# Optimization experiments

Measured on AMD Instinct MI355X. Metric: run time of the kernel, lower is better.

Reference implementation:

```python
import jax, jax.numpy as jnp
import numpy as np

N_NODES = 50000
N_EDGES = 800000
D_IN, HIDDEN, OUT, K = 96, 64, 16, 3


def _glorot(key, shape):
    fan_in, fan_out = shape[-2], shape[-1]
    lim = (6.0 / (fan_in + fan_out)) ** 0.5
    return jax.random.uniform(key, shape, jnp.float32, -lim, lim)


def setup_inputs() -> dict:
    key = jax.random.key(0)
    k1, k2, k3, k4 = jax.random.split(key, 4)
    x = jax.random.normal(k1, (N_NODES, D_IN), dtype=jnp.float32)
    edge_index = jax.random.randint(k2, (2, N_EDGES), 0, N_NODES, dtype=jnp.int64)
    # ChebConv params: K stacked linear maps per layer + one bias per layer
    W1 = _glorot(k3, (K, D_IN, HIDDEN))
    b1 = jnp.zeros((HIDDEN,), jnp.float32)
    W2 = _glorot(k4, (K, HIDDEN, OUT))
    b2 = jnp.zeros((OUT,), jnp.float32)
    return {"x": x, "edge_index": edge_index, "W1": W1, "b1": b1, "W2": W2, "b2": b2}


def _cheb_norm(edge_index, num_nodes):
    # PyG ChebConv norm with normalization='sym', lambda_max=2.0:
    # Ltilde = (2/lmax)*(I - D^-1/2 A D^-1/2) - I = -D^-1/2 A D^-1/2 (diag weight 0)
    src, dst = edge_index[0], edge_index[1]
    ones = jnp.ones((edge_index.shape[1],), jnp.float32)
    deg = jax.ops.segment_sum(ones, src, num_segments=num_nodes)
    dis = jnp.where(deg > 0, jax.lax.rsqrt(jnp.maximum(deg, 1.0)), 0.0)
    return -dis[src] * dis[dst]  # [E]


def _cheb_conv(x, src, dst, w, W, b, num_nodes):
    # Chebyshev recurrence: Tx0=x, Tx1=L x, Txk=2 L Tx_{k-1} - Tx_{k-2}
    def prop(h):  # sparse matvec: scatter-add of weighted source features
        return jax.ops.segment_sum(w[:, None] * h[src], dst, num_segments=num_nodes)

    Tx0 = x
    out = Tx0 @ W[0]
    Tx1 = prop(Tx0)
    out = out + Tx1 @ W[1]
    for k in range(2, W.shape[0]):
        Tx2 = 2.0 * prop(Tx1) - Tx0
        out = out + Tx2 @ W[k]
        Tx0, Tx1 = Tx1, Tx2
    return out + b


def reference(x, edge_index, W1, b1, W2, b2):
    num_nodes = x.shape[0]
    src, dst = edge_index[0], edge_index[1]
    w = _cheb_norm(edge_index, num_nodes)
    h = jax.nn.relu(_cheb_conv(x, src, dst, w, W1, b1, num_nodes))
    return _cheb_conv(h, src, dst, w, W2, b2, num_nodes)
```

## Files before the change

kernel.cpp:

```cpp
#include <hip/hip_runtime.h>

#define N_NODES 50000
#define N_EDGES 800000
#define D_IN 96
#define HID 64
#define D_OUT 16

#define EPB 2048
#define NBLK_E ((N_EDGES + EPB - 1) / EPB)
#define BSHIFT 7
#define NBKT ((N_NODES + 127) / 128)
#define DCAP 2560
#define PACK_TOT (3 * D_IN * HID + 3 * HID * D_OUT)
#define PACK_BLKS (PACK_TOT / 256)
#define GEMM1_BLKS ((N_NODES / 16 + 3) / 4)

typedef unsigned short u16;
typedef unsigned int u32;
typedef __attribute__((ext_vector_type(4))) float f32x4;
typedef __attribute__((ext_vector_type(8))) short bf16x8;

__device__ inline float bflo(u32 v) { union { u32 i; float f; } u; u.i = v << 16; return u.f; }
__device__ inline float bfhi(u32 v) { union { u32 i; float f; } u; u.i = v & 0xffff0000u; return u.f; }
__device__ inline u16 f2bf(float f) {
    union { float f; u32 i; } u; u.f = f;
    return (u16)((u.i + 0x7fffu + ((u.i >> 16) & 1u)) >> 16);
}
__device__ inline u32 pack2(float lo, float hi) {
    return (u32)f2bf(lo) | ((u32)f2bf(hi) << 16);
}


__global__ __launch_bounds__(256)
void passA(const int* __restrict__ src, const int* __restrict__ dst,
           int* __restrict__ blk_cnt_src, int* __restrict__ blk_cnt_dst,
           const float* __restrict__ W1, const float* __restrict__ W2,
           u16* __restrict__ Pb1, u16* __restrict__ Pb2) {
    const int t = threadIdx.x, blk = blockIdx.x;
    if (blk >= NBLK_E) {
        int tt = (blk - NBLK_E) * 256 + t;
        if (tt < 3 * D_IN * HID) {
            int j = tt & 7, rest = tt >> 3;
            int c = rest % 192, i = (rest / 192) * 8 + j;
            int kc = c / 64, o = c % 64;
            Pb1[tt] = f2bf(W1[((long)kc * D_IN + i) * HID + o]);
        } else if (tt < PACK_TOT) {
            int t2 = tt - 3 * D_IN * HID;
            int j = t2 & 7, rest = t2 >> 3;
            int c = rest % 48, i = (rest / 48) * 8 + j;
            int kc = c / 16, o = c % 16;
            Pb2[t2] = f2bf(W2[((long)kc * HID + i) * D_OUT + o]);
        }
        return;
    }
    __shared__ int hs[NBKT], hd[NBKT];
    for (int i = t; i < NBKT; i += 256) { hs[i] = 0; hd[i] = 0; }
    __syncthreads();
    const int e0 = blk * EPB;
    const int e1 = (e0 + EPB < N_EDGES) ? e0 + EPB : N_EDGES;
    for (int e = e0 + t; e < e1; e += 256) {
        atomicAdd(&hs[src[e] >> BSHIFT], 1);
        atomicAdd(&hd[dst[e] >> BSHIFT], 1);
    }
    __syncthreads();
    for (int b = t; b < NBKT; b += 256) {
        blk_cnt_src[b * NBLK_E + blk] = hs[b];
        blk_cnt_dst[b * NBLK_E + blk] = hd[b];
    }
}

__global__ __launch_bounds__(64)
void passB(int* __restrict__ blk_cnt_src, int* __restrict__ blk_cnt_dst,
           int* __restrict__ tot_src, int* __restrict__ tot_dst) {
    const int b = blockIdx.x;
    int* cnt; int* tot;
    if (b < NBKT) { cnt = blk_cnt_dst + b * NBLK_E;          tot = tot_dst + b; }
    else          { cnt = blk_cnt_src + (b - NBKT) * NBLK_E; tot = tot_src + (b - NBKT); }
    const int lane = threadIdx.x;
    int carry = 0;
    for (int base0 = 0; base0 < NBLK_E; base0 += 64) {
        int i = base0 + lane;
        int v = (i < NBLK_E) ? cnt[i] : 0;
        int incl = v;
        #pragma unroll
        for (int off = 1; off < 64; off <<= 1) {
            int x = __shfl_up(incl, off);
            if (lane >= off) incl += x;
        }
        if (i < NBLK_E) cnt[i] = carry + incl - v;
        carry += __shfl(incl, 63);
    }
    if (lane == 0) *tot = carry;
}


template<int K, int NC, int LDZ, int CPK, bool AF32, bool SCALE>
__device__ __forceinline__
void gemm_body(int tile, int lane, const void* __restrict__ Av, const u16* sP,
               u16* __restrict__ D02, u16* __restrict__ Z1, u16* __restrict__ Z2out,
               const float* __restrict__ dis) {
    constexpr int KT = K / 32;
    const int node0 = tile * 16;
    const int sub = lane >> 4, r16 = lane & 15;
    float dis4[4];
    if constexpr (SCALE) {
        #pragma unroll
        for (int r = 0; r < 4; ++r) dis4[r] = dis[node0 + sub * 4 + r];
    }
    bf16x8 a[KT];
    if constexpr (AF32) {
        const float* ar = (const float*)Av + (long)(node0 + r16) * K + sub * 8;
        #pragma unroll
        for (int kt = 0; kt < KT; ++kt) {
            float4 a0 = *(const float4*)(ar + kt * 32);
            float4 a1 = *(const float4*)(ar + kt * 32 + 4);
            union { bf16x8 v; uint4 q; } u;
            u.q.x = pack2(a0.x, a0.y); u.q.y = pack2(a0.z, a0.w);
            u.q.z = pack2(a1.x, a1.y); u.q.w = pack2(a1.z, a1.w);
            a[kt] = u.v;
        }
    } else {
        const u16* ar = (const u16*)Av + (long)(node0 + r16) * K + sub * 8;
        #pragma unroll
        for (int kt = 0; kt < KT; ++kt)
            a[kt] = *(const bf16x8*)(ar + kt * 32);
    }
    auto cc = [&](int ct) {
        f32x4 acc = {0.f, 0.f, 0.f, 0.f};
        #pragma unroll
        for (int kt = 0; kt < KT; ++kt) {
            bf16x8 bfr = *(const bf16x8*)&sP[((kt * 4 + sub) * NC + ct * 16 + r16) * 8];
            acc = __builtin_amdgcn_mfma_f32_16x16x32_bf16(a[kt], bfr, acc, 0, 0, 0);
        }
        return acc;
    };
    #pragma unroll
    for (int i = 0; i < CPK; ++i) {
        f32x4 acc0 = cc(i);
        f32x4 acc2 = cc(2 * CPK + i);
        const long rowoff = (long)(node0 + sub * 4) * LDZ + i * 16 + r16;
        #pragma unroll
        for (int r = 0; r < 4; ++r) {
            D02[rowoff + (long)r * LDZ] = f2bf(acc0[r] - acc2[r]);
            Z2out[rowoff + (long)r * LDZ] = SCALE ? f2bf(acc2[r] * dis4[r]) : f2bf(acc2[r]);
        }
    }
    #pragma unroll
    for (int i = 0; i < CPK; ++i) {
        f32x4 acc1 = cc(CPK + i);
        const long rowoff = (long)(node0 + sub * 4) * LDZ + i * 16 + r16;
        #pragma unroll
        for (int r = 0; r < 4; ++r)
            Z1[rowoff + (long)r * LDZ] = f2bf(acc1[r]);
    }
}


__global__ __launch_bounds__(256)
void passC_gemm1(const int* __restrict__ src, const int* __restrict__ dst,
                 const int* __restrict__ blk_off_src, const int* __restrict__ blk_off_dst,
                 const int* __restrict__ tot_src, const int* __restrict__ tot_dst,
                 u16* __restrict__ sorted_srconly, u32* __restrict__ sorted_pair,
                 const float* __restrict__ x, const u16* __restrict__ Pb1,
                 u16* __restrict__ D02, u16* __restrict__ Z1, u16* __restrict__ Zs) {
    __shared__ __align__(16) char smem[36864];
    const int t = threadIdx.x, blk = blockIdx.x;
    if (blk >= NBLK_E) {
        u16* sP = (u16*)smem;
        for (int idx = t * 8; idx < D_IN * 192; idx += 2048)
            *(uint4*)&sP[idx] = *(const uint4*)&Pb1[idx];
        __syncthreads();
        const int tile = (blk - NBLK_E) * 4 + (t >> 6);
        if (tile * 16 >= N_NODES) return;
        gemm_body<D_IN, 192, HID, 4, true, false>(tile, t & 63, x, sP, D02, Z1, Zs, nullptr);
        return;
    }
    int* s  = (int*)smem;
    int* cs = s + 512;
    int* cd = cs + NBKT;
    for (int pass = 0; pass < 2; ++pass) {
        const int* tot = pass ? tot_src : tot_dst;
        const int* bo  = pass ? blk_off_src : blk_off_dst;
        int* cx = pass ? cs : cd;
        s[t]       = (t < NBKT) ? tot[t] : 0;
        s[t + 256] = (t + 256 < NBKT) ? tot[t + 256] : 0;
        __syncthreads();
        for (int off = 1; off < 512; off <<= 1) {
            int a1 = (t >= off) ? s[t - off] : 0;
            int a2 = (t + 256 >= off) ? s[t + 256 - off] : 0;
            __syncthreads();
            s[t] += a1; s[t + 256] += a2;
            __syncthreads();
        }
        if (t < NBKT) cx[t] = s[t] - tot[t] + bo[t * NBLK_E + blk];
        if (t + 256 < NBKT) cx[t + 256] = s[t + 256] - tot[t + 256] + bo[(t + 256) * NBLK_E + blk];
        __syncthreads();
    }
    const int e0 = blk * EPB;
    const int e1 = (e0 + EPB < N_EDGES) ? e0 + EPB : N_EDGES;
    for (int e = e0 + t; e < e1; e += 256) {
        int sv = src[e], dv = dst[e];
        int ps = atomicAdd(&cs[sv >> BSHIFT], 1);
        sorted_srconly[ps] = (u16)sv;
        int pd = atomicAdd(&cd[dv >> BSHIFT], 1);
        sorted_pair[pd] = ((u32)dv << 16) | (u32)sv;
    }
}

__global__ __launch_bounds__(256)
void passD(const int* __restrict__ tot_src, const u16* __restrict__ sorted_srconly,
           const int* __restrict__ tot_dst, const u32* __restrict__ sorted_pair,
           float* __restrict__ dis, int* __restrict__ row_ptr, u16* __restrict__ wsrc,
           u16* __restrict__ Zs) {
    __shared__ int sred[256];
    __shared__ int hist[128];
    __shared__ int cur[128];
    __shared__ float s_dis[128];
    __shared__ u32 s_p[DCAP];
    const int t = threadIdx.x;
    const bool isSrc = blockIdx.x < NBKT;
    const int b = isSrc ? blockIdx.x : blockIdx.x - NBKT;
    const int* tot = isSrc ? tot_src : tot_dst;
    int part = 0;
    for (int i = t; i < b; i += 256) part += tot[i];
    sred[t] = part;
    if (t < 128) hist[t] = 0;
    __syncthreads();
    #pragma unroll
    for (int off = 128; off > 0; off >>= 1) {
        if (t < off) sred[t] += sred[t + off];
        __syncthreads();
    }
    const int eb = sred[0];
    const int ee = eb + tot[b];
    if (isSrc) {
        for (int i = eb + t; i < ee; i += 256)
            atomicAdd(&hist[sorted_srconly[i] & 127], 1);
        __syncthreads();
        const int node0 = b << BSHIFT;
        if (t < 128) {
            int c = hist[t];
            float dv = c > 0 ? rsqrtf((float)c) : 0.0f;
            s_dis[t] = dv;
            if (node0 + t < N_NODES) dis[node0 + t] = dv;
        }
        __syncthreads();
        for (int c = t; c < 128 * 8; c += 256) {
            int ln = c >> 3, off8 = (c & 7) * 8;
            int n = node0 + ln;
            if (n >= N_NODES) continue;
            float dv = s_dis[ln];
            u16* zp = Zs + (long)n * HID + off8;
            uint4 q = *(uint4*)zp;
            uint4 r;
            r.x = pack2(bflo(q.x) * dv, bfhi(q.x) * dv);
            r.y = pack2(bflo(q.y) * dv, bfhi(q.y) * dv);
            r.z = pack2(bflo(q.z) * dv, bfhi(q.z) * dv);
            r.w = pack2(bflo(q.w) * dv, bfhi(q.w) * dv);
            *(uint4*)zp = r;
        }
        return;
    }
    if (b == 0 && t == 0) row_ptr[N_NODES] = N_EDGES;
    const int cnt = ee - eb;
    const int stage = cnt < DCAP ? cnt : DCAP;
    for (int i = t; i < stage; i += 256) {
        u32 v = sorted_pair[eb + i];
        s_p[i] = v;
        atomicAdd(&hist[(v >> 16) & 127], 1);
    }
    for (int i = stage + t; i < cnt; i += 256)
        atomicAdd(&hist[(sorted_pair[eb + i] >> 16) & 127], 1);
    __syncthreads();
    if (t < 64) {
        int v0 = hist[2 * t], v1 = hist[2 * t + 1];
        int p = v0 + v1;
        int incl = p;
        #pragma unroll
        for (int off = 1; off < 64; off <<= 1) {
            int x = __shfl_up(incl, off);
            if (t >= off) incl += x;
        }
        int excl = incl - p;
        cur[2 * t] = excl;
        cur[2 * t + 1] = excl + v0;
        int node = (b << BSHIFT) + 2 * t;
        if (node < N_NODES) row_ptr[node] = eb + excl;
        if (node + 1 < N_NODES) row_ptr[node + 1] = eb + excl + v0;
    }
    __syncthreads();
    for (int i = t; i < stage; i += 256) {
        u32 v = s_p[i];
        int slot = atomicAdd(&cur[(v >> 16) & 127], 1);
        wsrc[eb + slot] = (u16)(v & 0xFFFF);
    }
    for (int i = stage + t; i < cnt; i += 256) {
        u32 v = sorted_pair[eb + i];
        int slot = atomicAdd(&cur[(v >> 16) & 127], 1);
        wsrc[eb + slot] = (u16)(v & 0xFFFF);
    }
}


__global__ __launch_bounds__(256)
void gemm2_kernel(const u16* __restrict__ A, const u16* __restrict__ P,
                  u16* __restrict__ D02, u16* __restrict__ Z1, u16* __restrict__ Zs,
                  const float* __restrict__ dis) {
    __shared__ u16 sP[HID * 48];
    for (int idx = threadIdx.x * 8; idx < HID * 48; idx += 2048)
        *(uint4*)&sP[idx] = *(const uint4*)&P[idx];
    __syncthreads();
    const int tile = blockIdx.x * 4 + (threadIdx.x >> 6);
    if (tile * 16 >= N_NODES) return;
    gemm_body<HID, 48, D_OUT, 1, false, true>(tile, threadIdx.x & 63, A, sP, D02, Z1, Zs, dis);
}


#define EPI_S 0
#define EPI_H 1
#define EPI_OUT 2

__device__ inline void sum8(float (&acc)[8], uint4 q) {
    acc[0] += bflo(q.x); acc[1] += bfhi(q.x);
    acc[2] += bflo(q.y); acc[3] += bfhi(q.y);
    acc[4] += bflo(q.z); acc[5] += bfhi(q.z);
    acc[6] += bflo(q.w); acc[7] += bfhi(q.w);
}

template<int F, int FS, int NPB, int CAP, int EPI>
__global__ __launch_bounds__(256)
void gather_prop(const int* __restrict__ row_ptr, const u16* __restrict__ ws,
                 const u16* __restrict__ g,
                 const u16* __restrict__ aux1,
                 const float* __restrict__ bias,
                 const float* __restrict__ dis,
                 void* __restrict__ outp) {
    static_assert(NPB * (FS / 8) == 256, "block geometry");
    constexpr int SPLIT = F / FS;
    __shared__ u16 s_p[CAP];
    __shared__ int s_beg[NPB + 1];
    const int tid = threadIdx.x;
    const int nodeblk = blockIdx.x / SPLIT;
    const int half = blockIdx.x % SPLIT;
    const int node0 = nodeblk * NPB;
    if (tid <= NPB) {
        int n = node0 + tid;
        s_beg[tid] = row_ptr[n > N_NODES ? N_NODES : n];
    }
    __syncthreads();
    const int ebeg = s_beg[0];
    const int cnt = s_beg[NPB] - ebeg;
    const int stage = cnt < CAP ? cnt : CAP;
    for (int e = tid; e < stage; e += 256)
        s_p[e] = ws[ebeg + e];
    __syncthreads();
    constexpr int CPN = FS / 8;
    const int nl = tid / CPN;
    const int node = node0 + nl;
    if (node >= N_NODES) return;
    const int c8 = (tid % CPN) * 8 + half * FS;
    float acc[8];
    #pragma unroll
    for (int j = 0; j < 8; ++j) acc[j] = 0.0f;
    const int beg = s_beg[nl] - ebeg;
    const int end = s_beg[nl + 1] - ebeg;
    const int mid = end < stage ? end : stage;
    int e = beg;
    for (; e + 8 <= mid; e += 8) {
        int p0 = s_p[e],     p1 = s_p[e + 1], p2 = s_p[e + 2], p3 = s_p[e + 3];
        int p4 = s_p[e + 4], p5 = s_p[e + 5], p6 = s_p[e + 6], p7 = s_p[e + 7];
        uint4 q0 = *(const uint4*)(g + (long)p0 * F + c8);
        uint4 q1 = *(const uint4*)(g + (long)p1 * F + c8);
        uint4 q2 = *(const uint4*)(g + (long)p2 * F + c8);
        uint4 q3 = *(const uint4*)(g + (long)p3 * F + c8);
        uint4 q4 = *(const uint4*)(g + (long)p4 * F + c8);
        uint4 q5 = *(const uint4*)(g + (long)p5 * F + c8);
        uint4 q6 = *(const uint4*)(g + (long)p6 * F + c8);
        uint4 q7 = *(const uint4*)(g + (long)p7 * F + c8);
        sum8(acc, q0); sum8(acc, q1); sum8(acc, q2); sum8(acc, q3);
        sum8(acc, q4); sum8(acc, q5); sum8(acc, q6); sum8(acc, q7);
    }
    for (; e + 4 <= mid; e += 4) {
        int p0 = s_p[e], p1 = s_p[e + 1], p2 = s_p[e + 2], p3 = s_p[e + 3];
        uint4 q0 = *(const uint4*)(g + (long)p0 * F + c8);
        uint4 q1 = *(const uint4*)(g + (long)p1 * F + c8);
        uint4 q2 = *(const uint4*)(g + (long)p2 * F + c8);
        uint4 q3 = *(const uint4*)(g + (long)p3 * F + c8);
        sum8(acc, q0); sum8(acc, q1); sum8(acc, q2); sum8(acc, q3);
    }
    for (; e < mid; ++e)
        sum8(acc, *(const uint4*)(g + (long)s_p[e] * F + c8));
    for (e = (beg > stage ? beg : stage); e < end; ++e)
        sum8(acc, *(const uint4*)(g + (long)ws[ebeg + e] * F + c8));
    const float dd = dis[node];
    if (EPI == EPI_S) {
        const float m1 = dd, m2 = -2.0f * dd * dd;
        const uint4 z1 = *(const uint4*)(aux1 + (long)node * F + c8);
        uint4 r;
        r.x = pack2(fmaf(m1, bflo(z1.x), m2 * acc[0]), fmaf(m1, bfhi(z1.x), m2 * acc[1]));
        r.y = pack2(fmaf(m1, bflo(z1.y), m2 * acc[2]), fmaf(m1, bfhi(z1.y), m2 * acc[3]));
        r.z = pack2(fmaf(m1, bflo(z1.z), m2 * acc[4]), fmaf(m1, bfhi(z1.z), m2 * acc[5]));
        r.w = pack2(fmaf(m1, bflo(z1.w), m2 * acc[6]), fmaf(m1, bfhi(z1.w), m2 * acc[7]));
        *(uint4*)((u16*)outp + (long)node * F + c8) = r;
    } else {
        const uint4 z0 = *(const uint4*)(aux1 + (long)node * F + c8);
        const float* bb = bias + c8;
        float v0 = bflo(z0.x) - dd * acc[0] + bb[0];
        float v1 = bfhi(z0.x) - dd * acc[1] + bb[1];
        float v2 = bflo(z0.y) - dd * acc[2] + bb[2];
        float v3 = bfhi(z0.y) - dd * acc[3] + bb[3];
        float v4 = bflo(z0.z) - dd * acc[4] + bb[4];
        float v5 = bfhi(z0.z) - dd * acc[5] + bb[5];
        float v6 = bflo(z0.w) - dd * acc[6] + bb[6];
        float v7 = bfhi(z0.w) - dd * acc[7] + bb[7];
        if (EPI == EPI_H) {
            uint4 r;
            r.x = pack2(fmaxf(v0, 0.f), fmaxf(v1, 0.f));
            r.y = pack2(fmaxf(v2, 0.f), fmaxf(v3, 0.f));
            r.z = pack2(fmaxf(v4, 0.f), fmaxf(v5, 0.f));
            r.w = pack2(fmaxf(v6, 0.f), fmaxf(v7, 0.f));
            *(uint4*)((u16*)outp + (long)node * F + c8) = r;
        } else {
            float* op = (float*)outp + (long)node * F + c8;
            *(float4*)op = make_float4(v0, v1, v2, v3);
            *(float4*)(op + 4) = make_float4(v4, v5, v6, v7);
        }
    }
}


extern "C" void kernel_launch(void* const* d_in, const int* in_sizes, int n_in,
                              void* d_out, int out_size, void* d_ws, size_t ws_size,
                              hipStream_t stream) {
    const float* x  = (const float*)d_in[0];
    const int*   ei = (const int*)d_in[1];
    const float* W1 = (const float*)d_in[2];
    const float* b1 = (const float*)d_in[3];
    const float* W2 = (const float*)d_in[4];
    const float* b2 = (const float*)d_in[5];
    const int* src = ei;
    const int* dst = ei + N_EDGES;

    float* dis          = (float*)d_ws;
    int*   row_ptr      = (int*)(dis + N_NODES);
    int*   blk_cnt_src  = row_ptr + 50016;
    int*   blk_cnt_dst  = blk_cnt_src + 152896;
    int*   tot_src      = blk_cnt_dst + 152896;
    int*   tot_dst      = tot_src + 512;
    u16*   srconly      = (u16*)(tot_dst + 512);
    u32*   sorted_pair  = (u32*)(srconly + N_EDGES);
    u16*   wsrc         = (u16*)(sorted_pair + N_EDGES);
    u16*   D02          = wsrc + N_EDGES;
    u16*   Z1b          = D02 + (long)N_NODES * HID;
    u16*   Zs           = Z1b + (long)N_NODES * HID;
    u16*   S            = Zs  + (long)N_NODES * HID;
    u16*   hb           = S   + (long)N_NODES * HID;
    u16*   D02p         = hb  + (long)N_NODES * HID;
    u16*   Z1p          = D02p + (long)N_NODES * D_OUT;
    u16*   Zsp          = Z1p  + (long)N_NODES * D_OUT;
    u16*   Sp           = Zsp  + (long)N_NODES * D_OUT;
    u16*   Pb1          = Sp   + (long)N_NODES * D_OUT;
    u16*   Pb2          = Pb1 + 18432;

    passA<<<NBLK_E + PACK_BLKS, 256, 0, stream>>>(src, dst, blk_cnt_src, blk_cnt_dst,
                                                  W1, W2, Pb1, Pb2);
    passB<<<2 * NBKT, 64, 0, stream>>>(blk_cnt_src, blk_cnt_dst, tot_src, tot_dst);
    passC_gemm1<<<NBLK_E + GEMM1_BLKS, 256, 0, stream>>>(
        src, dst, blk_cnt_src, blk_cnt_dst, tot_src, tot_dst,
        srconly, sorted_pair, x, Pb1, D02, Z1b, Zs);
    passD<<<2 * NBKT, 256, 0, stream>>>(tot_src, srconly, tot_dst, sorted_pair,
                                        dis, row_ptr, wsrc, Zs);

    gather_prop<HID, 32, 64, 1536, EPI_S><<<2 * ((N_NODES + 63) / 64), 256, 0, stream>>>(
        row_ptr, wsrc, Zs, Z1b, nullptr, dis, S);
    gather_prop<HID, 32, 64, 1536, EPI_H><<<2 * ((N_NODES + 63) / 64), 256, 0, stream>>>(
        row_ptr, wsrc, S, D02, b1, dis, hb);

    gemm2_kernel<<<GEMM1_BLKS, 256, 0, stream>>>(hb, Pb2, D02p, Z1p, Zsp, dis);
    gather_prop<D_OUT, 16, 128, 3072, EPI_S><<<(N_NODES + 127) / 128, 256, 0, stream>>>(
        row_ptr, wsrc, Zsp, Z1p, nullptr, dis, Sp);
    gather_prop<D_OUT, 16, 128, 3072, EPI_OUT><<<(N_NODES + 127) / 128, 256, 0, stream>>>(
        row_ptr, wsrc, Sp, D02p, b2, dis, (float*)d_out);
}
```

Measured before the change: 120.5 us.

## Fuse second layer-1 propagation with ReLU and layer-2 GEMM via LDS tile

The gather that produces the ReLU hidden features now keeps each 32-node tile of h in shared memory and immediately runs the layer-2 MFMA GEMM on it, writing D02p/Z1p/Zsp directly. This removes the separate gemm2 kernel launch and the global write and read of the 50000x64 bf16 hidden tensor. In exchange the gather uses 32 nodes per block with all 64 features instead of 64 nodes split across two blocks, only two of four waves do the GEMM, and LDS use per block rises, which may lower occupancy.

Result: faster. 117.7 us (-2.4%).

```diff
diff --git a/kernel.cpp b/kernel.cpp
--- a/kernel.cpp
+++ b/kernel.cpp
@@ -94,19 +94,13 @@
 }
 
 
-template<int K, int NC, int LDZ, int CPK, bool AF32, bool SCALE>
+template<int K, int NC, int LDZ, int CPK, bool AF32>
 __device__ __forceinline__
 void gemm_body(int tile, int lane, const void* __restrict__ Av, const u16* sP,
-               u16* __restrict__ D02, u16* __restrict__ Z1, u16* __restrict__ Z2out,
-               const float* __restrict__ dis) {
+               u16* __restrict__ D02, u16* __restrict__ Z1, u16* __restrict__ Z2out) {
     constexpr int KT = K / 32;
     const int node0 = tile * 16;
     const int sub = lane >> 4, r16 = lane & 15;
-    float dis4[4];
-    if constexpr (SCALE) {
-        #pragma unroll
-        for (int r = 0; r < 4; ++r) dis4[r] = dis[node0 + sub * 4 + r];
-    }
     bf16x8 a[KT];
     if constexpr (AF32) {
         const float* ar = (const float*)Av + (long)(node0 + r16) * K + sub * 8;
@@ -142,7 +136,7 @@
         #pragma unroll
         for (int r = 0; r < 4; ++r) {
             D02[rowoff + (long)r * LDZ] = f2bf(acc0[r] - acc2[r]);
-            Z2out[rowoff + (long)r * LDZ] = SCALE ? f2bf(acc2[r] * dis4[r]) : f2bf(acc2[r]);
+            Z2out[rowoff + (long)r * LDZ] = f2bf(acc2[r]);
         }
     }
     #pragma unroll
@@ -172,7 +166,7 @@
         __syncthreads();
         const int tile = (blk - NBLK_E) * 4 + (t >> 6);
         if (tile * 16 >= N_NODES) return;
-        gemm_body<D_IN, 192, HID, 4, true, false>(tile, t & 63, x, sP, D02, Z1, Zs, nullptr);
+        gemm_body<D_IN, 192, HID, 4, true>(tile, t & 63, x, sP, D02, Z1, Zs);
         return;
     }
     int* s  = (int*)smem;
@@ -302,24 +296,6 @@
 }
 
 
-__global__ __launch_bounds__(256)
-void gemm2_kernel(const u16* __restrict__ A, const u16* __restrict__ P,
-                  u16* __restrict__ D02, u16* __restrict__ Z1, u16* __restrict__ Zs,
-                  const float* __restrict__ dis) {
-    __shared__ u16 sP[HID * 48];
-    for (int idx = threadIdx.x * 8; idx < HID * 48; idx += 2048)
-        *(uint4*)&sP[idx] = *(const uint4*)&P[idx];
-    __syncthreads();
-    const int tile = blockIdx.x * 4 + (threadIdx.x >> 6);
-    if (tile * 16 >= N_NODES) return;
-    gemm_body<HID, 48, D_OUT, 1, false, true>(tile, threadIdx.x & 63, A, sP, D02, Z1, Zs, dis);
-}
-
-
-#define EPI_S 0
-#define EPI_H 1
-#define EPI_OUT 2
-
 __device__ inline void sum8(float (&acc)[8], uint4 q) {
     acc[0] += bflo(q.x); acc[1] += bfhi(q.x);
     acc[2] += bflo(q.y); acc[3] += bfhi(q.y);
@@ -327,44 +303,10 @@
     acc[6] += bflo(q.w); acc[7] += bfhi(q.w);
 }
 
-template<int F, int FS, int NPB, int CAP, int EPI>
-__global__ __launch_bounds__(256)
-void gather_prop(const int* __restrict__ row_ptr, const u16* __restrict__ ws,
-                 const u16* __restrict__ g,
-                 const u16* __restrict__ aux1,
-                 const float* __restrict__ bias,
-                 const float* __restrict__ dis,
-                 void* __restrict__ outp) {
-    static_assert(NPB * (FS / 8) == 256, "block geometry");
-    constexpr int SPLIT = F / FS;
-    __shared__ u16 s_p[CAP];
-    __shared__ int s_beg[NPB + 1];
-    const int tid = threadIdx.x;
-    const int nodeblk = blockIdx.x / SPLIT;
-    const int half = blockIdx.x % SPLIT;
-    const int node0 = nodeblk * NPB;
-    if (tid <= NPB) {
-        int n = node0 + tid;
-        s_beg[tid] = row_ptr[n > N_NODES ? N_NODES : n];
-    }
-    __syncthreads();
-    const int ebeg = s_beg[0];
-    const int cnt = s_beg[NPB] - ebeg;
-    const int stage = cnt < CAP ? cnt : CAP;
-    for (int e = tid; e < stage; e += 256)
-        s_p[e] = ws[ebeg + e];
-    __syncthreads();
-    constexpr int CPN = FS / 8;
-    const int nl = tid / CPN;
-    const int node = node0 + nl;
-    if (node >= N_NODES) return;
-    const int c8 = (tid % CPN) * 8 + half * FS;
-    float acc[8];
-    #pragma unroll
-    for (int j = 0; j < 8; ++j) acc[j] = 0.0f;
-    const int beg = s_beg[nl] - ebeg;
-    const int end = s_beg[nl + 1] - ebeg;
-    const int mid = end < stage ? end : stage;
+template<int F>
+__device__ __forceinline__
+void gather_loop(float (&acc)[8], const u16* s_p, const u16* ws, const u16* g,
+                 int beg, int mid, int end, int stage, int ebeg, int c8) {
     int e = beg;
     for (; e + 8 <= mid; e += 8) {
         int p0 = s_p[e],     p1 = s_p[e + 1], p2 = s_p[e + 2], p3 = s_p[e + 3];
@@ -392,6 +334,49 @@
         sum8(acc, *(const uint4*)(g + (long)s_p[e] * F + c8));
     for (e = (beg > stage ? beg : stage); e < end; ++e)
         sum8(acc, *(const uint4*)(g + (long)ws[ebeg + e] * F + c8));
+}
+
+
+#define EPI_S 0
+#define EPI_OUT 2
+
+template<int F, int FS, int NPB, int CAP, int EPI>
+__global__ __launch_bounds__(256)
+void gather_prop(const int* __restrict__ row_ptr, const u16* __restrict__ ws,
+                 const u16* __restrict__ g, const u16* __restrict__ aux1,
+                 const float* __restrict__ bias, const float* __restrict__ dis,
+                 void* __restrict__ outp) {
+    static_assert(NPB * (FS / 8) == 256, "block geometry");
+    constexpr int SPLIT = F / FS;
+    __shared__ u16 s_p[CAP];
+    __shared__ int s_beg[NPB + 1];
+    const int tid = threadIdx.x;
+    const int nodeblk = blockIdx.x / SPLIT;
+    const int half = blockIdx.x % SPLIT;
+    const int node0 = nodeblk * NPB;
+    if (tid <= NPB) {
+        int n = node0 + tid;
+        s_beg[tid] = row_ptr[n > N_NODES ? N_NODES : n];
+    }
+    __syncthreads();
+    const int ebeg = s_beg[0];
+    const int cnt = s_beg[NPB] - ebeg;
+    const int stage = cnt < CAP ? cnt : CAP;
+    for (int e = tid; e < stage; e += 256)
+        s_p[e] = ws[ebeg + e];
+    __syncthreads();
+    constexpr int CPN = FS / 8;
+    const int nl = tid / CPN;
+    const int node = node0 + nl;
+    if (node >= N_NODES) return;
+    const int c8 = (tid % CPN) * 8 + half * FS;
+    float acc[8];
+    #pragma unroll
+    for (int j = 0; j < 8; ++j) acc[j] = 0.0f;
+    const int beg = s_beg[nl] - ebeg;
+    const int end = s_beg[nl + 1] - ebeg;
+    const int mid = end < stage ? end : stage;
+    gather_loop<F>(acc, s_p, ws, g, beg, mid, end, stage, ebeg, c8);
     const float dd = dis[node];
     if (EPI == EPI_S) {
         const float m1 = dd, m2 = -2.0f * dd * dd;
@@ -413,18 +398,101 @@
         float v5 = bfhi(z0.z) - dd * acc[5] + bb[5];
         float v6 = bflo(z0.w) - dd * acc[6] + bb[6];
         float v7 = bfhi(z0.w) - dd * acc[7] + bb[7];
-        if (EPI == EPI_H) {
-            uint4 r;
-            r.x = pack2(fmaxf(v0, 0.f), fmaxf(v1, 0.f));
-            r.y = pack2(fmaxf(v2, 0.f), fmaxf(v3, 0.f));
-            r.z = pack2(fmaxf(v4, 0.f), fmaxf(v5, 0.f));
-            r.w = pack2(fmaxf(v6, 0.f), fmaxf(v7, 0.f));
-            *(uint4*)((u16*)outp + (long)node * F + c8) = r;
-        } else {
-            float* op = (float*)outp + (long)node * F + c8;
-            *(float4*)op = make_float4(v0, v1, v2, v3);
-            *(float4*)(op + 4) = make_float4(v4, v5, v6, v7);
-        }
+        float* op = (float*)outp + (long)node * F + c8;
+        *(float4*)op = make_float4(v0, v1, v2, v3);
+        *(float4*)(op + 4) = make_float4(v4, v5, v6, v7);
+    }
+}
+
+
+__global__ __launch_bounds__(256)
+void prop2_gemm2(const int* __restrict__ row_ptr, const u16* __restrict__ ws,
+                 const u16* __restrict__ S, const u16* __restrict__ D02,
+                 const float* __restrict__ b1, const float* __restrict__ dis,
+                 const u16* __restrict__ Pb2,
+                 u16* __restrict__ D02p, u16* __restrict__ Z1p, u16* __restrict__ Zsp) {
+    constexpr int NPB = 32, CAP = 1280;
+    __shared__ u16 s_p[CAP];
+    __shared__ int s_beg[NPB + 1];
+    __shared__ u16 sP[HID * 48];
+    __shared__ u16 h_tile[NPB][HID + 8];
+    const int tid = threadIdx.x;
+    const int node0 = blockIdx.x * NPB;
+    for (int idx = tid * 8; idx < HID * 48; idx += 2048)
+        *(uint4*)&sP[idx] = *(const uint4*)&Pb2[idx];
+    if (tid <= NPB) {
+        int n = node0 + tid;
+        s_beg[tid] = row_ptr[n > N_NODES ? N_NODES : n];
+    }
+    __syncthreads();
+    const int ebeg = s_beg[0];
+    const int cnt = s_beg[NPB] - ebeg;
+    const int stage = cnt < CAP ? cnt : CAP;
+    for (int e = tid; e < stage; e += 256)
+        s_p[e] = ws[ebeg + e];
+    __syncthreads();
+    const int nl = tid >> 3;
+    const int node = node0 + nl;
+    const int c8 = (tid & 7) * 8;
+    if (node < N_NODES) {
+        float acc[8];
+        #pragma unroll
+        for (int j = 0; j < 8; ++j) acc[j] = 0.0f;
+        const int beg = s_beg[nl] - ebeg;
+        const int end = s_beg[nl + 1] - ebeg;
+        const int mid = end < stage ? end : stage;
+        gather_loop<HID>(acc, s_p, ws, S, beg, mid, end, stage, ebeg, c8);
+        const float dd = dis[node];
+        const uint4 z0 = *(const uint4*)(D02 + (long)node * HID + c8);
+        const float* bb = b1 + c8;
+        float v0 = bflo(z0.x) - dd * acc[0] + bb[0];
+        float v1 = bfhi(z0.x) - dd * acc[1] + bb[1];
+        float v2 = bflo(z0.y) - dd * acc[2] + bb[2];
+        float v3 = bfhi(z0.y) - dd * acc[3] + bb[3];
+        float v4 = bflo(z0.z) - dd * acc[4] + bb[4];
+        float v5 = bfhi(z0.z) - dd * acc[5] + bb[5];
+        float v6 = bflo(z0.w) - dd * acc[6] + bb[6];
+        float v7 = bfhi(z0.w) - dd * acc[7] + bb[7];
+        uint4 r;
+        r.x = pack2(fmaxf(v0, 0.f), fmaxf(v1, 0.f));
+        r.y = pack2(fmaxf(v2, 0.f), fmaxf(v3, 0.f));
+        r.z = pack2(fmaxf(v4, 0.f), fmaxf(v5, 0.f));
+        r.w = pack2(fmaxf(v6, 0.f), fmaxf(v7, 0.f));
+        *(uint4*)&h_tile[nl][c8] = r;
+    }
+    __syncthreads();
+    const int w = tid >> 6;
+    if (w >= 2) return;
+    const int tile = blockIdx.x * 2 + w;
+    if (tile * 16 >= N_NODES) return;
+    const int lane = tid & 63;
+    const int sub = lane >> 4, r16 = lane & 15;
+    const int gnode0 = tile * 16;
+    float dis4[4];
+    #pragma unroll
+    for (int r = 0; r < 4; ++r) dis4[r] = dis[gnode0 + sub * 4 + r];
+    bf16x8 a[2];
+    const u16* ar = &h_tile[w * 16 + r16][sub * 8];
+    a[0] = *(const bf16x8*)(ar);
+    a[1] = *(const bf16x8*)(ar + 32);
+    auto cc = [&](int ct) {
+        f32x4 acc = {0.f, 0.f, 0.f, 0.f};
+        #pragma unroll
+        for (int kt = 0; kt < 2; ++kt) {
+            bf16x8 bfr = *(const bf16x8*)&sP[((kt * 4 + sub) * 48 + ct * 16 + r16) * 8];
+            acc = __builtin_amdgcn_mfma_f32_16x16x32_bf16(a[kt], bfr, acc, 0, 0, 0);
+        }
+        return acc;
+    };
+    f32x4 acc0 = cc(0);
+    f32x4 acc2 = cc(2);
+    f32x4 acc1 = cc(1);
+    const long rowoff = (long)(gnode0 + sub * 4) * D_OUT + r16;
+    #pragma unroll
+    for (int r = 0; r < 4; ++r) {
+        D02p[rowoff + (long)r * D_OUT] = f2bf(acc0[r] - acc2[r]);
+        Zsp[rowoff + (long)r * D_OUT]  = f2bf(acc2[r] * dis4[r]);
+        Z1p[rowoff + (long)r * D_OUT]  = f2bf(acc1[r]);
     }
 }
 
@@ -454,8 +522,7 @@
     u16*   Z1b          = D02 + (long)N_NODES * HID;
     u16*   Zs           = Z1b + (long)N_NODES * HID;
     u16*   S            = Zs  + (long)N_NODES * HID;
-    u16*   hb           = S   + (long)N_NODES * HID;
-    u16*   D02p         = hb  + (long)N_NODES * HID;
+    u16*   D02p         = S   + (long)N_NODES * HID;
     u16*   Z1p          = D02p + (long)N_NODES * D_OUT;
     u16*   Zsp          = Z1p  + (long)N_NODES * D_OUT;
     u16*   Sp           = Zsp  + (long)N_NODES * D_OUT;
@@ -473,10 +540,9 @@
 
     gather_prop<HID, 32, 64, 1536, EPI_S><<<2 * ((N_NODES + 63) / 64), 256, 0, stream>>>(
         row_ptr, wsrc, Zs, Z1b, nullptr, dis, S);
-    gather_prop<HID, 32, 64, 1536, EPI_H><<<2 * ((N_NODES + 63) / 64), 256, 0, stream>>>(
-        row_ptr, wsrc, S, D02, b1, dis, hb);
-
-    gemm2_kernel<<<GEMM1_BLKS, 256, 0, stream>>>(hb, Pb2, D02p, Z1p, Zsp, dis);
+    prop2_gemm2<<<(N_NODES + 31) / 32, 256, 0, stream>>>(
+        row_ptr, wsrc, S, D02, b1, dis, Pb2, D02p, Z1p, Zsp);
+
     gather_prop<D_OUT, 16, 128, 3072, EPI_S><<<(N_NODES + 127) / 128, 256, 0, stream>>>(
         row_ptr, wsrc, Zsp, Z1p, nullptr, dis, Sp);
     gather_prop<D_OUT, 16, 128, 3072, EPI_OUT><<<(N_NODES + 127) / 128, 256, 0, stream>>>(
```
